# Optimization experiments

Measured on AMD Instinct MI355X. Metric: run time of the kernel, lower is better.

The kernel has to match this reference:

```python
import jax, jax.numpy as jnp
import numpy as np

N, H, R, E = 100000, 128, 30, 600000
EPS = 1e-5  # BatchNorm1d default eps


def _rgcn_layer(h, src, dst, etype, W, root, bias):
    """PyG RGCNConv: out = h @ root + bias + sum_r scatter_mean_r(h[src] @ W[r]).
    Mean is per (dst, relation) edge count."""
    n = h.shape[0]
    r_count = W.shape[0]
    seg = dst * r_count + etype                      # combined (dst, rel) segment id
    deg = jax.ops.segment_sum(jnp.ones_like(etype, dtype=h.dtype), seg,
                              num_segments=n * r_count)
    norm = 1.0 / jnp.maximum(deg[seg], 1.0)          # (E,) per-edge mean weight

    def body(out, inp):
        Wr, r = inp
        xr = h @ Wr                                  # (N,H) relation-transformed feats
        contrib = jnp.where((etype == r)[:, None], xr[src] * norm[:, None], 0.0)
        return out + jax.ops.segment_sum(contrib, dst, num_segments=n), None

    out0 = h @ root + bias
    out, _ = jax.lax.scan(body, out0, (W, jnp.arange(r_count)))
    return out


def _bn_relu(h, gamma, beta):
    # BatchNorm1d in training mode: biased batch statistics over the node dim
    mu = h.mean(axis=0)
    var = h.var(axis=0)
    return jax.nn.relu((h - mu) * jax.lax.rsqrt(var + EPS) * gamma + beta)


def setup_inputs() -> dict:
    key = jax.random.key(0)
    ks = jax.random.split(key, 16)
    s = 1.0 / np.sqrt(H)
    return {
        "x": jnp.arange(N, dtype=jnp.int32),
        "edge_index": jax.random.randint(ks[0], (2, E), 0, N, dtype=jnp.int32),
        "edge_type": jax.random.randint(ks[1], (E,), 0, R, dtype=jnp.int32),
        "emb": jax.random.normal(ks[2], (N, H), jnp.float32) * s,
        "W1": jax.random.normal(ks[3], (R, H, H), jnp.float32) * s,
        "root1": jax.random.normal(ks[4], (H, H), jnp.float32) * s,
        "b1": jnp.zeros((H,), jnp.float32),
        "g1": jnp.ones((H,), jnp.float32),
        "be1": jnp.zeros((H,), jnp.float32),
        "W2": jax.random.normal(ks[5], (R, H, H), jnp.float32) * s,
        "root2": jax.random.normal(ks[6], (H, H), jnp.float32) * s,
        "b2": jnp.zeros((H,), jnp.float32),
        "g2": jnp.ones((H,), jnp.float32),
        "be2": jnp.zeros((H,), jnp.float32),
    }


def reference(x, edge_index, edge_type, emb, W1, root1, b1, g1, be1,
              W2, root2, b2, g2, be2):
    src, dst = edge_index[0], edge_index[1]
    h = emb[x]                                        # (N,H) embedding lookup
    h = _bn_relu(_rgcn_layer(h, src, dst, edge_type, W1, root1, b1), g1, be1)
    h = _bn_relu(_rgcn_layer(h, src, dst, edge_type, W2, root2, b2), g2, be2)
    return h  # dropout is identity (deterministic reference)
```

## Files before the change

kernel.cpp:

```cpp
#include <hip/hip_runtime.h>
#include <hip/hip_bf16.h>

#define NN 100000
#define HH 128
#define RR 30
#define NE 600000
#define TILE 64
#define CH 64
#define EPAD (NE + RR * TILE)
#define NB_PS ((NN + 255) / 256)
#define NBLK_BN 784
#define RPB_BN 128
#define BN_EPS 1e-5f

typedef __bf16 v8bf __attribute__((ext_vector_type(8)));
typedef float  v4f  __attribute__((ext_vector_type(4)));

static __device__ __forceinline__ unsigned short f2b(float f) {
    unsigned int u = __float_as_uint(f);
    unsigned int r = (u + 0x7FFF + ((u >> 16) & 1)) >> 16;
    return (unsigned short)r;
}

__global__ void k_hist(const int* __restrict__ dst, const int* __restrict__ et,
                       int* __restrict__ deg, int* __restrict__ cnt,
                       int* __restrict__ cnt_dst) {
    __shared__ int lh[RR];
    int t = threadIdx.x;
    if (t < RR) lh[t] = 0;
    __syncthreads();
    int i = blockIdx.x * blockDim.x + t;
    if (i < NE) {
        int d = dst[i], r = et[i];
        atomicAdd(&deg[d * RR + r], 1);
        atomicAdd(&cnt_dst[d], 1);
        atomicAdd(&lh[r], 1);
    }
    __syncthreads();
    if (t < RR && lh[t]) atomicAdd(&cnt[t], lh[t]);
}

__global__ void k_scan(const int* __restrict__ cnt, int* __restrict__ cursor,
                       int* __restrict__ totals,
                       int* __restrict__ src_s, int* __restrict__ dst_s,
                       int* __restrict__ et_s, float* __restrict__ norm_s,
                       int* __restrict__ dpos_s) {
    __shared__ int off[RR + 1];
    if (threadIdx.x == 0) {
        int acc = 0;
        for (int r = 0; r < RR; ++r) {
            off[r] = acc;
            acc += (cnt[r] + TILE - 1) / TILE;
        }
        off[RR] = acc;
        totals[0] = acc * TILE;
    }
    __syncthreads();
    for (int r = 0; r < RR; ++r) {
        int begin = off[r] * TILE + cnt[r];
        int end   = off[r + 1] * TILE;
        for (int p = begin + (int)threadIdx.x; p < end; p += blockDim.x) {
            src_s[p] = 0; dst_s[p] = 0; et_s[p] = r; norm_s[p] = 0.f;
            dpos_s[p] = NE;
        }
    }
    if (threadIdx.x == 0)
        for (int r = 0; r < RR; ++r) cursor[r] = off[r] * TILE;
}

__global__ void k_psum1(const int* __restrict__ c, int* __restrict__ bsum) {
    __shared__ int sh[256];
    int i = blockIdx.x * 256 + threadIdx.x;
    sh[threadIdx.x] = (i < NN) ? c[i] : 0;
    __syncthreads();
    for (int s = 128; s > 0; s >>= 1) {
        if (threadIdx.x < s) sh[threadIdx.x] += sh[threadIdx.x + s];
        __syncthreads();
    }
    if (threadIdx.x == 0) bsum[blockIdx.x] = sh[0];
}

__global__ void k_psum2(int* __restrict__ bsum) {
    __shared__ int sh[512];
    int t = threadIdx.x;
    sh[t] = (t < NB_PS) ? bsum[t] : 0;
    __syncthreads();
    if (t == 0) {
        int acc = 0;
        for (int b = 0; b < NB_PS; ++b) { int v = sh[b]; sh[b] = acc; acc += v; }
    }
    __syncthreads();
    if (t < NB_PS) bsum[t] = sh[t];
}

__global__ void k_psum3(const int* __restrict__ c, const int* __restrict__ bscan,
                        int* __restrict__ off, int* __restrict__ cur) {
    __shared__ int sh[256];
    int t = threadIdx.x;
    int i = blockIdx.x * 256 + t;
    int v = (i < NN) ? c[i] : 0;
    sh[t] = v;
    __syncthreads();
    for (int s = 1; s < 256; s <<= 1) {
        int a = (t >= s) ? sh[t - s] : 0;
        __syncthreads();
        sh[t] += a;
        __syncthreads();
    }
    int excl = sh[t] - v + bscan[blockIdx.x];
    if (i < NN) { off[i] = excl; cur[i] = excl; }
    if (i == 0) off[NN] = NE;
}

__global__ void k_scatter(const int* __restrict__ src, const int* __restrict__ dst,
                          const int* __restrict__ et, const int* __restrict__ deg,
                          int* __restrict__ cursor, int* __restrict__ cursor_dst,
                          int* __restrict__ src_s, int* __restrict__ dst_s,
                          int* __restrict__ et_s, float* __restrict__ norm_s,
                          int* __restrict__ dpos_s, int* __restrict__ ds2) {
    __shared__ int lh[RR];
    __shared__ int lbase[RR];
    int t = threadIdx.x;
    if (t < RR) lh[t] = 0;
    __syncthreads();
    int i = blockIdx.x * blockDim.x + t;
    int r = 0, d = 0, lrank = 0;
    bool valid = (i < NE);
    if (valid) {
        r = et[i]; d = dst[i];
        lrank = atomicAdd(&lh[r], 1);
    }
    __syncthreads();
    if (t < RR && lh[t]) lbase[t] = atomicAdd(&cursor[t], lh[t]);
    __syncthreads();
    if (valid) {
        int pos = lbase[r] + lrank;
        src_s[pos] = src[i];
        dst_s[pos] = d;
        et_s[pos]  = r;
        int dg = deg[d * RR + r];
        norm_s[pos] = 1.0f / (float)(dg > 1 ? dg : 1);
        int dp = atomicAdd(&cursor_dst[d], 1);
        dpos_s[pos] = dp;
        ds2[dp] = d;
    }
}

__global__ void k_convW(const float* __restrict__ W, unsigned short* __restrict__ Wt,
                        int total) {
    int idx = blockIdx.x * blockDim.x + threadIdx.x;
    if (idx >= total) return;
    int m = idx / (HH * HH);
    int rem = idx % (HH * HH);
    int k = rem / HH, c = rem % HH;
    Wt[m * HH * HH + c * HH + k] = f2b(W[idx]);
}

__global__ void k_embed(const int* __restrict__ x, const float* __restrict__ emb,
                        unsigned short* __restrict__ hb) {
    int idx = blockIdx.x * blockDim.x + threadIdx.x;
    if (idx >= NN * HH) return;
    int i = idx / HH, j = idx % HH;
    hb[idx] = f2b(emb[x[i] * HH + j]);
}

__global__ __launch_bounds__(256) void k_rootgemm(const unsigned short* __restrict__ hb,
                                                  const unsigned short* __restrict__ rootT,
                                                  const float* __restrict__ bias,
                                                  float* __restrict__ tmp) {
    __shared__ __align__(16) unsigned short Xs[TILE][HH + 8];
    __shared__ __align__(16) unsigned short Ws[HH][HH + 8];
    int base = blockIdx.x * TILE;
    int t = threadIdx.x;

    {
        int l = t >> 2, lr = t & 3;
        int row = base + l;
        for (int i = 0; i < 4; ++i) {
            int g = lr + 4 * i;
            uint4 v = {0u, 0u, 0u, 0u};
            if (row < NN) v = *reinterpret_cast<const uint4*>(hb + (size_t)row * HH + g * 8);
            *reinterpret_cast<uint4*>(&Xs[l][g * 8]) = v;
        }
    }
    for (int i = 0; i < 8; ++i) {
        int idx = t + 256 * i;
        int row = idx >> 4, g = idx & 15;
        *reinterpret_cast<uint4*>(&Ws[row][g * 8]) =
            *reinterpret_cast<const uint4*>(rootT + row * HH + g * 8);
    }
    __syncthreads();

    int w = t >> 6, lane = t & 63;
    int lr16 = lane & 15, kg = lane >> 4;
    v4f acc[8];
    for (int n = 0; n < 8; ++n) acc[n] = (v4f){0.f, 0.f, 0.f, 0.f};
#pragma unroll
    for (int kk = 0; kk < 4; ++kk) {
        int k0 = kk * 32 + kg * 8;
        v8bf a = *reinterpret_cast<const v8bf*>(&Xs[w * 16 + lr16][k0]);
#pragma unroll
        for (int n = 0; n < 8; ++n) {
            v8bf b = *reinterpret_cast<const v8bf*>(&Ws[n * 16 + lr16][k0]);
            acc[n] = __builtin_amdgcn_mfma_f32_16x16x32_bf16(a, b, acc[n], 0, 0, 0);
        }
    }
#pragma unroll
    for (int n = 0; n < 8; ++n)
        for (int j = 0; j < 4; ++j) {
            int row = base + w * 16 + kg * 4 + j;
            int col = n * 16 + lr16;
            if (row < NN) tmp[(size_t)row * HH + col] = acc[n][j] + bias[col];
        }
}

__global__ __launch_bounds__(256) void k_edgegemm_x(const unsigned short* __restrict__ hb,
                                                    const unsigned short* __restrict__ Wt,
                                                    const int* __restrict__ src_s,
                                                    const int* __restrict__ et_s,
                                                    const float* __restrict__ norm_s,
                                                    const int* __restrict__ dpos_s,
                                                    const int* __restrict__ totals,
                                                    unsigned short* __restrict__ xe) {
    int ebase = blockIdx.x * TILE;
    if (ebase >= totals[0]) return;
    __shared__ __align__(16) unsigned short Xs[TILE][HH + 8];
    __shared__ __align__(16) unsigned short Ws[HH][HH + 8];
    __shared__ int   src_l[TILE];
    __shared__ int   dpos_l[TILE];
    __shared__ float nrm_l[TILE];
    int t = threadIdx.x;
    if (t < TILE) {
        src_l[t]  = src_s[ebase + t];
        dpos_l[t] = dpos_s[ebase + t];
        nrm_l[t]  = norm_s[ebase + t];
    }
    int rel = et_s[ebase];
    __syncthreads();

    {
        int l = t >> 2, lr = t & 3;
        int srow = src_l[l];
        for (int i = 0; i < 4; ++i) {
            int g = lr + 4 * i;
            *reinterpret_cast<uint4*>(&Xs[l][g * 8]) =
                *reinterpret_cast<const uint4*>(hb + (size_t)srow * HH + g * 8);
        }
    }
    const unsigned short* Wr = Wt + (size_t)rel * HH * HH;
    for (int i = 0; i < 8; ++i) {
        int idx = t + 256 * i;
        int row = idx >> 4, g = idx & 15;
        *reinterpret_cast<uint4*>(&Ws[row][g * 8]) =
            *reinterpret_cast<const uint4*>(Wr + row * HH + g * 8);
    }
    __syncthreads();

    int w = t >> 6, lane = t & 63;
    int lr16 = lane & 15, kg = lane >> 4;
    v4f acc[8];
    for (int n = 0; n < 8; ++n) acc[n] = (v4f){0.f, 0.f, 0.f, 0.f};
#pragma unroll
    for (int kk = 0; kk < 4; ++kk) {
        int k0 = kk * 32 + kg * 8;
        v8bf a = *reinterpret_cast<const v8bf*>(&Xs[w * 16 + lr16][k0]);
#pragma unroll
        for (int n = 0; n < 8; ++n) {
            v8bf b = *reinterpret_cast<const v8bf*>(&Ws[n * 16 + lr16][k0]);
            acc[n] = __builtin_amdgcn_mfma_f32_16x16x32_bf16(a, b, acc[n], 0, 0, 0);
        }
    }
    __syncthreads();
#pragma unroll
    for (int n = 0; n < 8; ++n)
        for (int j = 0; j < 4; ++j) {
            int slot = w * 16 + kg * 4 + j;
            Xs[slot][n * 16 + lr16] = f2b(acc[n][j] * nrm_l[slot]);
        }
    __syncthreads();
    {
        int l = t >> 2, lr = t & 3;
        size_t drow = (size_t)dpos_l[l];
        for (int i = 0; i < 4; ++i) {
            int g = lr + 4 * i;
            *reinterpret_cast<uint4*>(xe + drow * HH + g * 8) =
                *reinterpret_cast<uint4*>(&Xs[l][g * 8]);
        }
    }
}

__global__ __launch_bounds__(256) void k_edgegemm_at(const unsigned short* __restrict__ hb,
                                                     const unsigned short* __restrict__ Wt,
                                                     const int* __restrict__ src_s,
                                                     const int* __restrict__ dst_s,
                                                     const int* __restrict__ et_s,
                                                     const float* __restrict__ norm_s,
                                                     const int* __restrict__ totals,
                                                     float* __restrict__ tmp) {
    int ebase = blockIdx.x * TILE;
    if (ebase >= totals[0]) return;
    __shared__ __align__(16) unsigned short Xs[TILE][HH + 8];
    __shared__ __align__(16) unsigned short Ws[HH][HH + 8];
    __shared__ int   src_l[TILE];
    __shared__ int   dst_l[TILE];
    __shared__ float nrm_l[TILE];
    int t = threadIdx.x;
    if (t < TILE) {
        src_l[t] = src_s[ebase + t];
        dst_l[t] = dst_s[ebase + t];
        nrm_l[t] = norm_s[ebase + t];
    }
    int rel = et_s[ebase];
    __syncthreads();
    {
        int l = t >> 2, lr = t & 3;
        int srow = src_l[l];
        for (int i = 0; i < 4; ++i) {
            int g = lr + 4 * i;
            *reinterpret_cast<uint4*>(&Xs[l][g * 8]) =
                *reinterpret_cast<const uint4*>(hb + (size_t)srow * HH + g * 8);
        }
    }
    const unsigned short* Wr = Wt + (size_t)rel * HH * HH;
    for (int i = 0; i < 8; ++i) {
        int idx = t + 256 * i;
        int row = idx >> 4, g = idx & 15;
        *reinterpret_cast<uint4*>(&Ws[row][g * 8]) =
            *reinterpret_cast<const uint4*>(Wr + row * HH + g * 8);
    }
    __syncthreads();
    int w = t >> 6, lane = t & 63;
    int lr16 = lane & 15, kg = lane >> 4;
    v4f acc[8];
    for (int n = 0; n < 8; ++n) acc[n] = (v4f){0.f, 0.f, 0.f, 0.f};
#pragma unroll
    for (int kk = 0; kk < 4; ++kk) {
        int k0 = kk * 32 + kg * 8;
        v8bf a = *reinterpret_cast<const v8bf*>(&Xs[w * 16 + lr16][k0]);
#pragma unroll
        for (int n = 0; n < 8; ++n) {
            v8bf b = *reinterpret_cast<const v8bf*>(&Ws[n * 16 + lr16][k0]);
            acc[n] = __builtin_amdgcn_mfma_f32_16x16x32_bf16(a, b, acc[n], 0, 0, 0);
        }
    }
#pragma unroll
    for (int n = 0; n < 8; ++n)
        for (int j = 0; j < 4; ++j) {
            int slot = w * 16 + kg * 4 + j;
            int col  = n * 16 + lr16;
            atomicAdd(&tmp[(size_t)dst_l[slot] * HH + col], acc[n][j] * nrm_l[slot]);
        }
}

static __device__ __forceinline__ void flushseg(int d, float a0, float a1,
                                                int c0, int c1,
                                                const int* __restrict__ off,
                                                float* __restrict__ tmp, int lane) {
    int s = off[d], e = off[d + 1];
    float* base = tmp + (size_t)d * HH + lane * 2;
    if (s >= c0 && e <= c1) {
        float2* b2 = reinterpret_cast<float2*>(base);
        float2 o = *b2; o.x += a0; o.y += a1; *b2 = o;
    } else {
        atomicAdd(base, a0);
        atomicAdd(base + 1, a1);
    }
}

__global__ __launch_bounds__(256) void k_aggseg(const unsigned int* __restrict__ xe32,
                                                const int* __restrict__ ds2,
                                                const int* __restrict__ off,
                                                float* __restrict__ tmp) {
    int wid = (blockIdx.x * blockDim.x + threadIdx.x) >> 6;
    int lane = threadIdx.x & 63;
    if (wid >= NE / CH) return;
    int c0 = wid * CH;

    int dme = ds2[c0 + lane];
    int dpre = __shfl_up(dme, 1);
    if (lane == 0) dpre = (c0 == 0) ? -1 : ds2[c0 - 1];
    unsigned long long bmask = __ballot(dme != dpre);

    int dcur = __shfl(dme, 0);
    float a0 = 0.f, a1 = 0.f;
    for (int q0 = 0; q0 < CH; q0 += 8) {
        unsigned int v[8];
#pragma unroll
        for (int j = 0; j < 8; ++j)
            v[j] = xe32[(size_t)(c0 + q0 + j) * 64 + lane];
#pragma unroll
        for (int j = 0; j < 8; ++j) {
            int q = q0 + j;
            if (q && ((bmask >> q) & 1ull)) {
                flushseg(dcur, a0, a1, c0, c0 + CH, off, tmp, lane);
                a0 = 0.f; a1 = 0.f;
                dcur = __shfl(dme, q);
            }
            a0 += __uint_as_float(v[j] << 16);
            a1 += __uint_as_float(v[j] & 0xffff0000u);
        }
    }
    flushseg(dcur, a0, a1, c0, c0 + CH, off, tmp, lane);
}

__global__ __launch_bounds__(256) void k_bnsum1(const float* __restrict__ tmp,
                                                float* __restrict__ psum,
                                                float* __restrict__ psq) {
    int t = threadIdx.x;
    int rg = t >> 5, lane = t & 31;
    int base = blockIdx.x * RPB_BN;
    v4f s = {0.f, 0.f, 0.f, 0.f}, q = {0.f, 0.f, 0.f, 0.f};
#pragma unroll 4
    for (int i = 0; i < RPB_BN / 8; ++i) {
        int row = base + rg + 8 * i;
        if (row < NN) {
            v4f v = *reinterpret_cast<const v4f*>(tmp + (size_t)row * HH + lane * 4);
            s += v; q += v * v;
        }
    }
    __shared__ v4f shs[8][32], shq[8][32];
    shs[rg][lane] = s; shq[rg][lane] = q;
    __syncthreads();
    if (rg == 0) {
        v4f ts = shs[0][lane], tq = shq[0][lane];
#pragma unroll
        for (int k = 1; k < 8; ++k) { ts += shs[k][lane]; tq += shq[k][lane]; }
        int b = blockIdx.x;
#pragma unroll
        for (int j = 0; j < 4; ++j) {
            psum[(size_t)(lane * 4 + j) * NBLK_BN + b] = ts[j];
            psq [(size_t)(lane * 4 + j) * NBLK_BN + b] = tq[j];
        }
    }
}

__global__ void k_bnsum2(const float* __restrict__ psum, const float* __restrict__ psq,
                         const float* __restrict__ g, const float* __restrict__ be,
                         float* __restrict__ sc_g, float* __restrict__ shf_g) {
    __shared__ float ssum[HH], ssq[HH];
    int t = threadIdx.x;
    int col = t & 127;
    const float* row = ((t < 128) ? psum : psq) + (size_t)col * NBLK_BN;
    v4f a = {0.f, 0.f, 0.f, 0.f};
    for (int i = 0; i < NBLK_BN / 4; ++i)
        a += *reinterpret_cast<const v4f*>(row + i * 4);
    float acc = a[0] + a[1] + a[2] + a[3];
    if (t < 128) ssum[col] = acc; else ssq[col] = acc;
    __syncthreads();
    if (t < 128) {
        float inv_n = 1.0f / (float)NN;
        float mean = ssum[col] * inv_n;
        float var = ssq[col] * inv_n - mean * mean;
        float sc = g[col] * rsqrtf(var + BN_EPS);
        sc_g[col] = sc;
        shf_g[col] = be[col] - mean * sc;
    }
}

__global__ void k_bnapply(const float* __restrict__ tmp, const float* __restrict__ sc_g,
                          const float* __restrict__ shf_g,
                          unsigned short* __restrict__ hout,
                          float* __restrict__ fout, int write_bf16) {
    int idx = blockIdx.x * blockDim.x + threadIdx.x;
    if (idx >= NN * HH / 4) return;
    int c4 = (idx & 31) * 4;
    v4f v  = *reinterpret_cast<const v4f*>(tmp + (size_t)idx * 4);
    v4f sc = *reinterpret_cast<const v4f*>(sc_g + c4);
    v4f sh = *reinterpret_cast<const v4f*>(shf_g + c4);
    v4f r;
#pragma unroll
    for (int j = 0; j < 4; ++j) r[j] = fmaxf(v[j] * sc[j] + sh[j], 0.f);
    if (write_bf16) {
        uint2 u;
        u.x = (unsigned int)f2b(r[0]) | ((unsigned int)f2b(r[1]) << 16);
        u.y = (unsigned int)f2b(r[2]) | ((unsigned int)f2b(r[3]) << 16);
        *reinterpret_cast<uint2*>(hout + (size_t)idx * 4) = u;
    } else {
        *reinterpret_cast<v4f*>(fout + (size_t)idx * 4) = r;
    }
}

constexpr size_t OFF_DEG  = 0;
constexpr size_t OFF_HB   = OFF_DEG + (size_t)NN * RR * 4;
constexpr size_t OFF_TMP  = OFF_HB + (size_t)NN * HH * 2;
constexpr size_t OFF_W1T  = OFF_TMP + (size_t)NN * HH * 4;
constexpr size_t OFF_W2T  = OFF_W1T + (size_t)RR * HH * HH * 2;
constexpr size_t OFF_R1T  = OFF_W2T + (size_t)RR * HH * HH * 2;
constexpr size_t OFF_R2T  = OFF_R1T + (size_t)HH * HH * 2;
constexpr size_t OFF_SRCS = OFF_R2T + (size_t)HH * HH * 2;
constexpr size_t OFF_DSTS = OFF_SRCS + (size_t)EPAD * 4;
constexpr size_t OFF_ETS  = OFF_DSTS + (size_t)EPAD * 4;
constexpr size_t OFF_NRMS = OFF_ETS + (size_t)EPAD * 4;
constexpr size_t OFF_DPOS = OFF_NRMS + (size_t)EPAD * 4;
constexpr size_t OFF_DS2  = OFF_DPOS + (size_t)EPAD * 4;
constexpr size_t OFF_CNTD = OFF_DS2 + (size_t)EPAD * 4;
constexpr size_t OFF_OFFD = OFF_CNTD + ((size_t)(NN + 1) * 4 + 255 & ~(size_t)255);
constexpr size_t OFF_CURD = OFF_OFFD + ((size_t)(NN + 1) * 4 + 255 & ~(size_t)255);
constexpr size_t OFF_BSUM = OFF_CURD + ((size_t)NN * 4 + 255 & ~(size_t)255);
constexpr size_t OFF_CTRL = OFF_BSUM + ((size_t)NB_PS * 4 + 255 & ~(size_t)255);
constexpr size_t OFF_SC   = OFF_CTRL + 512;
constexpr size_t OFF_SHF  = OFF_SC + 512;
constexpr size_t OFF_PSUM = OFF_SHF + 512;
constexpr size_t OFF_PSQ  = OFF_PSUM + (size_t)HH * NBLK_BN * 4;
constexpr size_t OFF_XE   = (OFF_PSQ + (size_t)HH * NBLK_BN * 4 + 255) & ~(size_t)255;
constexpr size_t WS_MIN   = OFF_XE;
constexpr size_t WS_FULL  = OFF_XE + (size_t)EPAD * HH * 2;

extern "C" void kernel_launch(void* const* d_in, const int* in_sizes, int n_in,
                              void* d_out, int out_size, void* d_ws, size_t ws_size,
                              hipStream_t stream) {
    const int*   x     = (const int*)d_in[0];
    const int*   eidx  = (const int*)d_in[1];
    const int*   et    = (const int*)d_in[2];
    const float* emb   = (const float*)d_in[3];
    const float* W1    = (const float*)d_in[4];
    const float* root1 = (const float*)d_in[5];
    const float* b1    = (const float*)d_in[6];
    const float* g1    = (const float*)d_in[7];
    const float* be1   = (const float*)d_in[8];
    const float* W2    = (const float*)d_in[9];
    const float* root2 = (const float*)d_in[10];
    const float* b2    = (const float*)d_in[11];
    const float* g2    = (const float*)d_in[12];
    const float* be2   = (const float*)d_in[13];
    float* out = (float*)d_out;

    if (ws_size < WS_MIN) return;
    const bool full = (ws_size >= WS_FULL);

    char* ws = (char*)d_ws;
    int*   deg    = (int*)(ws + OFF_DEG);
    unsigned short* hb = (unsigned short*)(ws + OFF_HB);
    float* tmp    = (float*)(ws + OFF_TMP);
    unsigned short* W1t = (unsigned short*)(ws + OFF_W1T);
    unsigned short* W2t = (unsigned short*)(ws + OFF_W2T);
    unsigned short* r1t = (unsigned short*)(ws + OFF_R1T);
    unsigned short* r2t = (unsigned short*)(ws + OFF_R2T);
    int*   src_s  = (int*)(ws + OFF_SRCS);
    int*   dst_s  = (int*)(ws + OFF_DSTS);
    int*   et_s   = (int*)(ws + OFF_ETS);
    float* norm_s = (float*)(ws + OFF_NRMS);
    int*   dpos_s = (int*)(ws + OFF_DPOS);
    int*   ds2    = (int*)(ws + OFF_DS2);
    int*   cnt_d  = (int*)(ws + OFF_CNTD);
    int*   off_d  = (int*)(ws + OFF_OFFD);
    int*   cur_d  = (int*)(ws + OFF_CURD);
    int*   bsum   = (int*)(ws + OFF_BSUM);
    int*   cnt    = (int*)(ws + OFF_CTRL);
    int*   cursor = cnt + 32;
    int*   totals = cnt + 64;
    float* sc_g   = (float*)(ws + OFF_SC);
    float* shf_g  = (float*)(ws + OFF_SHF);
    float* psum   = (float*)(ws + OFF_PSUM);
    float* psq    = (float*)(ws + OFF_PSQ);
    unsigned short* xe = (unsigned short*)(ws + OFF_XE);

    const int* srcp = eidx;
    const int* dstp = eidx + NE;

    hipMemsetAsync(deg, 0, (size_t)NN * RR * 4, stream);
    hipMemsetAsync(cnt, 0, 512, stream);
    hipMemsetAsync(cnt_d, 0, (size_t)(NN + 1) * 4, stream);

    k_hist<<<(NE + 255) / 256, 256, 0, stream>>>(dstp, et, deg, cnt, cnt_d);
    k_scan<<<1, 256, 0, stream>>>(cnt, cursor, totals, src_s, dst_s, et_s, norm_s, dpos_s);
    k_psum1<<<NB_PS, 256, 0, stream>>>(cnt_d, bsum);
    k_psum2<<<1, 512, 0, stream>>>(bsum);
    k_psum3<<<NB_PS, 256, 0, stream>>>(cnt_d, bsum, off_d, cur_d);
    k_scatter<<<(NE + 255) / 256, 256, 0, stream>>>(srcp, dstp, et, deg, cursor, cur_d,
                                                    src_s, dst_s, et_s, norm_s, dpos_s, ds2);
    k_convW<<<(RR * HH * HH + 255) / 256, 256, 0, stream>>>(W1, W1t, RR * HH * HH);
    k_convW<<<(RR * HH * HH + 255) / 256, 256, 0, stream>>>(W2, W2t, RR * HH * HH);
    k_convW<<<(HH * HH + 255) / 256, 256, 0, stream>>>(root1, r1t, HH * HH);
    k_convW<<<(HH * HH + 255) / 256, 256, 0, stream>>>(root2, r2t, HH * HH);
    k_embed<<<(NN * HH + 255) / 256, 256, 0, stream>>>(x, emb, hb);

    const unsigned short* Wts[2] = {W1t, W2t};
    const unsigned short* rts[2] = {r1t, r2t};
    const float* biases[2] = {b1, b2};
    const float* gs[2]     = {g1, g2};
    const float* bes[2]    = {be1, be2};

    const int nchunks = NE / CH;
    for (int layer = 0; layer < 2; ++layer) {
        k_rootgemm<<<(NN + TILE - 1) / TILE, 256, 0, stream>>>(hb, rts[layer],
                                                               biases[layer], tmp);
        if (full) {
            k_edgegemm_x<<<EPAD / TILE, 256, 0, stream>>>(hb, Wts[layer], src_s, et_s,
                                                          norm_s, dpos_s, totals, xe);
            k_aggseg<<<(nchunks + 3) / 4, 256, 0, stream>>>((const unsigned int*)xe,
                                                            ds2, off_d, tmp);
        } else {
            k_edgegemm_at<<<EPAD / TILE, 256, 0, stream>>>(hb, Wts[layer], src_s, dst_s,
                                                           et_s, norm_s, totals, tmp);
        }
        k_bnsum1<<<NBLK_BN, 256, 0, stream>>>(tmp, psum, psq);
        k_bnsum2<<<1, 256, 0, stream>>>(psum, psq, gs[layer], bes[layer], sc_g, shf_g);
        k_bnapply<<<(NN * HH / 4 + 255) / 256, 256, 0, stream>>>(tmp, sc_g, shf_g,
                                                                 hb, out, layer == 0);
    }
}
```

Before: 582.1 us.

## Trim preprocessing atomics and arrays; simplify segment flush in aggregation

Per-destination counts are now computed by summing the per-(dst,rel) degree table, so the extra atomic in the histogram goes away. The destination map ds2 is filled from the offsets instead of written by scatter. The per-edge relation array is replaced by a per-tile relation table, and dst_s is written only when the fallback path needs it. The aggregation kernel no longer reads offsets to decide between atomic and plain stores; it uses the boundary ballot plus the next chunk's destination instead, and it loads 16 rows per batch. Together these cut global traffic and atomics in setup and the reduce, at the cost of two more small kernel launches.

```diff
diff --git a/kernel.cpp b/kernel.cpp
--- a/kernel.cpp
+++ b/kernel.cpp
@@ -8,6 +8,7 @@
 #define TILE 64
 #define CH 64
 #define EPAD (NE + RR * TILE)
+#define NCHMAX (EPAD / TILE)
 #define NB_PS ((NN + 255) / 256)
 #define NBLK_BN 784
 #define RPB_BN 128
@@ -23,8 +24,7 @@
 }
 
 __global__ void k_hist(const int* __restrict__ dst, const int* __restrict__ et,
-                       int* __restrict__ deg, int* __restrict__ cnt,
-                       int* __restrict__ cnt_dst) {
+                       int* __restrict__ deg, int* __restrict__ cnt) {
     __shared__ int lh[RR];
     int t = threadIdx.x;
     if (t < RR) lh[t] = 0;
@@ -33,18 +33,26 @@
     if (i < NE) {
         int d = dst[i], r = et[i];
         atomicAdd(&deg[d * RR + r], 1);
-        atomicAdd(&cnt_dst[d], 1);
         atomicAdd(&lh[r], 1);
     }
     __syncthreads();
     if (t < RR && lh[t]) atomicAdd(&cnt[t], lh[t]);
+}
+
+__global__ void k_degsum(const int* __restrict__ deg, int* __restrict__ cnt_d) {
+    int d = blockIdx.x * blockDim.x + threadIdx.x;
+    if (d >= NN) return;
+    int s = 0;
+#pragma unroll
+    for (int r = 0; r < RR; ++r) s += deg[(size_t)d * RR + r];
+    cnt_d[d] = s;
 }
 
 __global__ void k_scan(const int* __restrict__ cnt, int* __restrict__ cursor,
                        int* __restrict__ totals,
                        int* __restrict__ src_s, int* __restrict__ dst_s,
-                       int* __restrict__ et_s, float* __restrict__ norm_s,
-                       int* __restrict__ dpos_s) {
+                       float* __restrict__ norm_s, int* __restrict__ dpos_s,
+                       int* __restrict__ chunk_rel, int need_dst) {
     __shared__ int off[RR + 1];
     if (threadIdx.x == 0) {
         int acc = 0;
@@ -57,11 +65,14 @@
     }
     __syncthreads();
     for (int r = 0; r < RR; ++r) {
+        for (int c = off[r] + (int)threadIdx.x; c < off[r + 1]; c += blockDim.x)
+            chunk_rel[c] = r;
         int begin = off[r] * TILE + cnt[r];
         int end   = off[r + 1] * TILE;
         for (int p = begin + (int)threadIdx.x; p < end; p += blockDim.x) {
-            src_s[p] = 0; dst_s[p] = 0; et_s[p] = r; norm_s[p] = 0.f;
+            src_s[p] = 0; norm_s[p] = 0.f;
             dpos_s[p] = NE;
+            if (need_dst) dst_s[p] = 0;
         }
     }
     if (threadIdx.x == 0)
@@ -112,12 +123,19 @@
     if (i == 0) off[NN] = NE;
 }
 
+__global__ void k_fillds2(const int* __restrict__ off, int* __restrict__ ds2) {
+    int d = blockIdx.x * blockDim.x + threadIdx.x;
+    if (d >= NN) return;
+    int s = off[d], e = off[d + 1];
+    for (int p = s; p < e; ++p) ds2[p] = d;
+}
+
 __global__ void k_scatter(const int* __restrict__ src, const int* __restrict__ dst,
                           const int* __restrict__ et, const int* __restrict__ deg,
                           int* __restrict__ cursor, int* __restrict__ cursor_dst,
                           int* __restrict__ src_s, int* __restrict__ dst_s,
-                          int* __restrict__ et_s, float* __restrict__ norm_s,
-                          int* __restrict__ dpos_s, int* __restrict__ ds2) {
+                          float* __restrict__ norm_s, int* __restrict__ dpos_s,
+                          int need_dst) {
     __shared__ int lh[RR];
     __shared__ int lbase[RR];
     int t = threadIdx.x;
@@ -136,13 +154,10 @@
     if (valid) {
         int pos = lbase[r] + lrank;
         src_s[pos] = src[i];
-        dst_s[pos] = d;
-        et_s[pos]  = r;
+        if (need_dst) dst_s[pos] = d;
         int dg = deg[d * RR + r];
         norm_s[pos] = 1.0f / (float)(dg > 1 ? dg : 1);
-        int dp = atomicAdd(&cursor_dst[d], 1);
-        dpos_s[pos] = dp;
-        ds2[dp] = d;
+        dpos_s[pos] = atomicAdd(&cursor_dst[d], 1);
     }
 }
 
@@ -217,7 +232,7 @@
 __global__ __launch_bounds__(256) void k_edgegemm_x(const unsigned short* __restrict__ hb,
                                                     const unsigned short* __restrict__ Wt,
                                                     const int* __restrict__ src_s,
-                                                    const int* __restrict__ et_s,
+                                                    const int* __restrict__ chunk_rel,
                                                     const float* __restrict__ norm_s,
                                                     const int* __restrict__ dpos_s,
                                                     const int* __restrict__ totals,
@@ -235,7 +250,7 @@
         dpos_l[t] = dpos_s[ebase + t];
         nrm_l[t]  = norm_s[ebase + t];
     }
-    int rel = et_s[ebase];
+    int rel = chunk_rel[blockIdx.x];
     __syncthreads();
 
     {
@@ -293,7 +308,7 @@
                                                      const unsigned short* __restrict__ Wt,
                                                      const int* __restrict__ src_s,
                                                      const int* __restrict__ dst_s,
-                                                     const int* __restrict__ et_s,
+                                                     const int* __restrict__ chunk_rel,
                                                      const float* __restrict__ norm_s,
                                                      const int* __restrict__ totals,
                                                      float* __restrict__ tmp) {
@@ -310,7 +325,7 @@
         dst_l[t] = dst_s[ebase + t];
         nrm_l[t] = norm_s[ebase + t];
     }
-    int rel = et_s[ebase];
+    int rel = chunk_rel[blockIdx.x];
     __syncthreads();
     {
         int l = t >> 2, lr = t & 3;
@@ -352,24 +367,8 @@
         }
 }
 
-static __device__ __forceinline__ void flushseg(int d, float a0, float a1,
-                                                int c0, int c1,
-                                                const int* __restrict__ off,
-                                                float* __restrict__ tmp, int lane) {
-    int s = off[d], e = off[d + 1];
-    float* base = tmp + (size_t)d * HH + lane * 2;
-    if (s >= c0 && e <= c1) {
-        float2* b2 = reinterpret_cast<float2*>(base);
-        float2 o = *b2; o.x += a0; o.y += a1; *b2 = o;
-    } else {
-        atomicAdd(base, a0);
-        atomicAdd(base + 1, a1);
-    }
-}
-
 __global__ __launch_bounds__(256) void k_aggseg(const unsigned int* __restrict__ xe32,
                                                 const int* __restrict__ ds2,
-                                                const int* __restrict__ off,
                                                 float* __restrict__ tmp) {
     int wid = (blockIdx.x * blockDim.x + threadIdx.x) >> 6;
     int lane = threadIdx.x & 63;
@@ -380,27 +379,47 @@
     int dpre = __shfl_up(dme, 1);
     if (lane == 0) dpre = (c0 == 0) ? -1 : ds2[c0 - 1];
     unsigned long long bmask = __ballot(dme != dpre);
+    int dnext = (c0 + CH < NE) ? ds2[c0 + CH] : -1;
 
     int dcur = __shfl(dme, 0);
+    bool fresh = (bmask & 1ull) != 0;
     float a0 = 0.f, a1 = 0.f;
-    for (int q0 = 0; q0 < CH; q0 += 8) {
-        unsigned int v[8];
-#pragma unroll
-        for (int j = 0; j < 8; ++j)
+    for (int q0 = 0; q0 < CH; q0 += 16) {
+        unsigned int v[16];
+#pragma unroll
+        for (int j = 0; j < 16; ++j)
             v[j] = xe32[(size_t)(c0 + q0 + j) * 64 + lane];
 #pragma unroll
-        for (int j = 0; j < 8; ++j) {
+        for (int j = 0; j < 16; ++j) {
             int q = q0 + j;
             if (q && ((bmask >> q) & 1ull)) {
-                flushseg(dcur, a0, a1, c0, c0 + CH, off, tmp, lane);
+                float* base = tmp + (size_t)dcur * HH + lane * 2;
+                if (fresh) {
+                    float2* b2 = reinterpret_cast<float2*>(base);
+                    float2 o = *b2; o.x += a0; o.y += a1; *b2 = o;
+                } else {
+                    atomicAdd(base, a0);
+                    atomicAdd(base + 1, a1);
+                }
                 a0 = 0.f; a1 = 0.f;
                 dcur = __shfl(dme, q);
+                fresh = true;
             }
             a0 += __uint_as_float(v[j] << 16);
             a1 += __uint_as_float(v[j] & 0xffff0000u);
         }
     }
-    flushseg(dcur, a0, a1, c0, c0 + CH, off, tmp, lane);
+    {
+        bool endclean = (dnext != dcur);
+        float* base = tmp + (size_t)dcur * HH + lane * 2;
+        if (fresh && endclean) {
+            float2* b2 = reinterpret_cast<float2*>(base);
+            float2 o = *b2; o.x += a0; o.y += a1; *b2 = o;
+        } else {
+            atomicAdd(base, a0);
+            atomicAdd(base + 1, a1);
+        }
+    }
 }
 
 __global__ __launch_bounds__(256) void k_bnsum1(const float* __restrict__ tmp,
@@ -489,11 +508,11 @@
 constexpr size_t OFF_R2T  = OFF_R1T + (size_t)HH * HH * 2;
 constexpr size_t OFF_SRCS = OFF_R2T + (size_t)HH * HH * 2;
 constexpr size_t OFF_DSTS = OFF_SRCS + (size_t)EPAD * 4;
-constexpr size_t OFF_ETS  = OFF_DSTS + (size_t)EPAD * 4;
-constexpr size_t OFF_NRMS = OFF_ETS + (size_t)EPAD * 4;
+constexpr size_t OFF_NRMS = OFF_DSTS + (size_t)EPAD * 4;
 constexpr size_t OFF_DPOS = OFF_NRMS + (size_t)EPAD * 4;
 constexpr size_t OFF_DS2  = OFF_DPOS + (size_t)EPAD * 4;
-constexpr size_t OFF_CNTD = OFF_DS2 + (size_t)EPAD * 4;
+constexpr size_t OFF_CREL = OFF_DS2 + (size_t)EPAD * 4;
+constexpr size_t OFF_CNTD = OFF_CREL + ((size_t)NCHMAX * 4 + 255 & ~(size_t)255);
 constexpr size_t OFF_OFFD = OFF_CNTD + ((size_t)(NN + 1) * 4 + 255 & ~(size_t)255);
 constexpr size_t OFF_CURD = OFF_OFFD + ((size_t)(NN + 1) * 4 + 255 & ~(size_t)255);
 constexpr size_t OFF_BSUM = OFF_CURD + ((size_t)NN * 4 + 255 & ~(size_t)255);
@@ -527,6 +546,7 @@
 
     if (ws_size < WS_MIN) return;
     const bool full = (ws_size >= WS_FULL);
+    const int need_dst = full ? 0 : 1;
 
     char* ws = (char*)d_ws;
     int*   deg    = (int*)(ws + OFF_DEG);
@@ -538,10 +558,10 @@
     unsigned short* r2t = (unsigned short*)(ws + OFF_R2T);
     int*   src_s  = (int*)(ws + OFF_SRCS);
     int*   dst_s  = (int*)(ws + OFF_DSTS);
-    int*   et_s   = (int*)(ws + OFF_ETS);
     float* norm_s = (float*)(ws + OFF_NRMS);
     int*   dpos_s = (int*)(ws + OFF_DPOS);
     int*   ds2    = (int*)(ws + OFF_DS2);
+    int*   crel   = (int*)(ws + OFF_CREL);
     int*   cnt_d  = (int*)(ws + OFF_CNTD);
     int*   off_d  = (int*)(ws + OFF_OFFD);
     int*   cur_d  = (int*)(ws + OFF_CURD);
@@ -560,15 +580,18 @@
 
     hipMemsetAsync(deg, 0, (size_t)NN * RR * 4, stream);
     hipMemsetAsync(cnt, 0, 512, stream);
-    hipMemsetAsync(cnt_d, 0, (size_t)(NN + 1) * 4, stream);
-
-    k_hist<<<(NE + 255) / 256, 256, 0, stream>>>(dstp, et, deg, cnt, cnt_d);
-    k_scan<<<1, 256, 0, stream>>>(cnt, cursor, totals, src_s, dst_s, et_s, norm_s, dpos_s);
+
+    k_hist<<<(NE + 255) / 256, 256, 0, stream>>>(dstp, et, deg, cnt);
+    k_degsum<<<(NN + 255) / 256, 256, 0, stream>>>(deg, cnt_d);
+    k_scan<<<1, 256, 0, stream>>>(cnt, cursor, totals, src_s, dst_s, norm_s,
+                                  dpos_s, crel, need_dst);
     k_psum1<<<NB_PS, 256, 0, stream>>>(cnt_d, bsum);
     k_psum2<<<1, 512, 0, stream>>>(bsum);
     k_psum3<<<NB_PS, 256, 0, stream>>>(cnt_d, bsum, off_d, cur_d);
+    k_fillds2<<<(NN + 255) / 256, 256, 0, stream>>>(off_d, ds2);
     k_scatter<<<(NE + 255) / 256, 256, 0, stream>>>(srcp, dstp, et, deg, cursor, cur_d,
-                                                    src_s, dst_s, et_s, norm_s, dpos_s, ds2);
+                                                    src_s, dst_s, norm_s, dpos_s,
+                                                    need_dst);
     k_convW<<<(RR * HH * HH + 255) / 256, 256, 0, stream>>>(W1, W1t, RR * HH * HH);
     k_convW<<<(RR * HH * HH + 255) / 256, 256, 0, stream>>>(W2, W2t, RR * HH * HH);
     k_convW<<<(HH * HH + 255) / 256, 256, 0, stream>>>(root1, r1t, HH * HH);
@@ -586,13 +609,13 @@
         k_rootgemm<<<(NN + TILE - 1) / TILE, 256, 0, stream>>>(hb, rts[layer],
                                                                biases[layer], tmp);
         if (full) {
-            k_edgegemm_x<<<EPAD / TILE, 256, 0, stream>>>(hb, Wts[layer], src_s, et_s,
+            k_edgegemm_x<<<EPAD / TILE, 256, 0, stream>>>(hb, Wts[layer], src_s, crel,
                                                           norm_s, dpos_s, totals, xe);
             k_aggseg<<<(nchunks + 3) / 4, 256, 0, stream>>>((const unsigned int*)xe,
-                                                            ds2, off_d, tmp);
+                                                            ds2, tmp);
         } else {
             k_edgegemm_at<<<EPAD / TILE, 256, 0, stream>>>(hb, Wts[layer], src_s, dst_s,
-                                                           et_s, norm_s, totals, tmp);
+                                                           crel, norm_s, totals, tmp);
         }
         k_bnsum1<<<NBLK_BN, 256, 0, stream>>>(tmp, psum, psq);
         k_bnsum2<<<1, 256, 0, stream>>>(psum, psq, gs[layer], bes[layer], sc_g, shf_g);
```

After: 536.5 us. -7.8%, faster.
